# Optimization experiments

Hardware: AMD Instinct MI355X
Metric: run time of the kernel (lower is better)

The kernel has to match this reference:

```python
import jax, jax.numpy as jnp
import numpy as np

MARGIN = 0.2
W_HARD = 1.0
W_SOFT = 0.0
NORMALIZE = True
PD_EPS = 1e-6  # torch F.pairwise_distance eps used inside TripletMarginLoss


def setup_inputs() -> dict:
    key = jax.random.key(0)
    k1, k2, k3 = jax.random.split(key, 3)
    N, D = 8192, 128
    z = jax.random.normal(k1, (N, D), dtype=jnp.float32)
    labels = jax.random.randint(k2, (N,), 0, 16, dtype=jnp.int32)
    subjects = jax.random.randint(k3, (N,), 0, 32, dtype=jnp.int32)
    return {"z": z, "labels": labels, "subjects": subjects}


def _batch_hard(z, pos_mask, neg_mask, margin):
    # pairwise euclidean distances (cdist p=2); mining indices are ints, so
    # stop_gradient keeps vjp clean (matches torch: argmax/argmin detach).
    sq = jnp.sum(z * z, axis=1)
    d2 = sq[:, None] + sq[None, :] - 2.0 * (z @ z.T)
    dist = jax.lax.stop_gradient(jnp.sqrt(jnp.maximum(d2, 0.0)))
    inf = jnp.asarray(jnp.inf, dist.dtype)
    p_idx = jnp.argmax(jnp.where(pos_mask, dist, -inf), axis=1)  # hardest positive
    n_idx = jnp.argmin(jnp.where(neg_mask, dist, inf), axis=1)   # hardest negative
    valid = jnp.any(pos_mask, axis=1) & jnp.any(neg_mask, axis=1)
    a, p, n = z, z[p_idx], z[n_idx]
    d_ap = jnp.sqrt(jnp.sum((a - p + PD_EPS) ** 2, axis=1))
    d_an = jnp.sqrt(jnp.sum((a - n + PD_EPS) ** 2, axis=1))
    per = jnp.maximum(d_ap - d_an + margin, 0.0)
    cnt = jnp.sum(valid)
    loss = jnp.sum(per * valid) / jnp.maximum(cnt, 1).astype(per.dtype)
    return jnp.where(cnt > 0, loss, 0.0)


def reference(z, labels, subjects):
    if NORMALIZE:
        z = z / jnp.maximum(jnp.linalg.norm(z, axis=1, keepdims=True), 1e-12)
    N = z.shape[0]
    same_class = labels[:, None] == labels[None, :]
    same_subj = subjects[:, None] == subjects[None, :]
    not_eye = ~jnp.eye(N, dtype=bool)
    loss = 0.0
    denom = 0.0
    if W_HARD != 0:
        pos_hard = same_class & ~same_subj & not_eye
        neg_hard = ~same_class & same_subj & not_eye
        loss = loss + W_HARD * _batch_hard(z, pos_hard, neg_hard, MARGIN)
        denom += abs(W_HARD)
    if W_SOFT != 0:
        pos_soft = same_class & same_subj & not_eye
        neg_soft = ~same_class & ~same_subj & not_eye
        loss = loss + W_SOFT * _batch_hard(z, pos_soft, neg_soft, MARGIN)
        denom += abs(W_SOFT)
    return loss / max(denom, 1e-12)
```

## Files before the change

### kernel.cpp

```cpp
#include <hip/hip_runtime.h>
#include <math.h>

#define N 8192
#define D 128
#define MARGIN 0.2f
#define PD_EPS 1e-6f
#define CLS_STRIDE 1024
#define SUB_STRIDE 512

typedef __attribute__((ext_vector_type(8))) short bf16x8;
typedef __attribute__((ext_vector_type(4))) float f32x4;

__device__ __forceinline__ unsigned short f2bf(float f) {
    unsigned u = __float_as_uint(f);
    u += 0x7FFFu + ((u >> 16) & 1u);
    return (unsigned short)(u >> 16);
}
__device__ __forceinline__ unsigned umn(unsigned a, unsigned b) { return a < b ? a : b; }
__device__ __forceinline__ unsigned umx(unsigned a, unsigned b) { return a > b ? a : b; }

__global__ __launch_bounds__(256) void k_normalize(const float* __restrict__ z,
                                                   unsigned short* __restrict__ znb,
                                                   float* __restrict__ invn) {
    int row  = blockIdx.x * 4 + (threadIdx.x >> 6);
    int lane = threadIdx.x & 63;
    float2 v = ((const float2*)(z + (size_t)row * D))[lane];
    float ss = v.x * v.x + v.y * v.y;
    #pragma unroll
    for (int m = 1; m < 64; m <<= 1) ss += __shfl_xor(ss, m, 64);
    float norm = fmaxf(sqrtf(ss), 1e-12f);
    ushort2 b; b.x = f2bf(v.x / norm); b.y = f2bf(v.y / norm);
    ((ushort2*)(znb + (size_t)row * D))[lane] = b;
    if (lane == 0) invn[row] = 1.0f / norm;
}

__global__ __launch_bounds__(1024) void k_bucket(const int* __restrict__ labels,
                                                 const int* __restrict__ subjects,
                                                 int* __restrict__ counters,
                                                 int* __restrict__ clsIdx,
                                                 int* __restrict__ subIdx,
                                                 float* __restrict__ acc) {
    __shared__ int hc[16], hs[32];
    const int t = threadIdx.x;
    if (t < 16) hc[t] = 0;
    if (t < 32) hs[t] = 0;
    if (t < 3)  acc[t] = 0.0f;
    __syncthreads();
    #pragma unroll
    for (int r = 0; r < 8; ++r) {
        int row = r * 1024 + t;
        int lab = labels[row], sub = subjects[row];
        int rc = atomicAdd(&hc[lab], 1);
        if (rc < CLS_STRIDE) clsIdx[lab * CLS_STRIDE + rc] = (sub << 13) | row;
        int rs = atomicAdd(&hs[sub], 1);
        if (rs < SUB_STRIDE) subIdx[sub * SUB_STRIDE + rs] = (lab << 13) | row;
    }
    __syncthreads();
    if (t < 16) counters[t] = hc[t];
    else if (t < 48) counters[t] = hs[t - 16];
}

__global__ __launch_bounds__(64, 2) void k_mine(const unsigned short* __restrict__ znb,
                                                const int* __restrict__ counters,
                                                const int* __restrict__ clsIdx,
                                                const int* __restrict__ subIdx,
                                                unsigned* __restrict__ posk,
                                                unsigned* __restrict__ negk) {
    const int b = blockIdx.x;
    const bool isPos = b < 256;
    const int* idx; int cnt, atile;
    if (isPos) {
        int c = b >> 4; atile = b & 15;
        idx = clsIdx + c * CLS_STRIDE;
        cnt = min(counters[c], CLS_STRIDE);
    } else {
        int t = b - 256; int su = t >> 3; atile = t & 7;
        idx = subIdx + su * SUB_STRIDE;
        cnt = min(counters[16 + su], SUB_STRIDE);
    }
    if (atile * 64 >= cnt) return;

    const int lane = threadIdx.x;
    const int m = lane & 15, quad = lane >> 4;

    bf16x8 afrag[4][4];
    #pragma unroll
    for (int u = 0; u < 4; ++u) {
        int sl = min(atile * 64 + u * 16 + m, cnt - 1);
        size_t row = (size_t)(idx[sl] & 8191);
        #pragma unroll
        for (int s = 0; s < 4; ++s)
            afrag[u][s] = *(const bf16x8*)(znb + row * D + s * 32 + quad * 8);
    }
    int cpk[16];
    #pragma unroll
    for (int u = 0; u < 4; ++u)
        #pragma unroll
        for (int r = 0; r < 4; ++r)
            cpk[u * 4 + r] = idx[min(atile * 64 + u * 16 + quad * 4 + r, cnt - 1)];

    unsigned best[16];
    #pragma unroll
    for (int s = 0; s < 16; ++s) best[s] = isPos ? 0xFFFFFFFFu : 0u;

    const int njt = (cnt + 63) >> 6;
    for (int t = 0; t < njt; ++t) {
        int pkB[4];
        #pragma unroll
        for (int v = 0; v < 4; ++v)
            pkB[v] = idx[min(t * 64 + v * 16 + m, cnt - 1)];

        f32x4 acc[4][4];
        #pragma unroll
        for (int u = 0; u < 4; ++u)
            #pragma unroll
            for (int v = 0; v < 4; ++v)
                acc[u][v] = (f32x4){0.f, 0.f, 0.f, 0.f};

        #pragma unroll
        for (int s = 0; s < 4; ++s) {
            bf16x8 bf[4];
            #pragma unroll
            for (int v = 0; v < 4; ++v)
                bf[v] = *(const bf16x8*)(znb + (size_t)(pkB[v] & 8191) * D + s * 32 + quad * 8);
            #pragma unroll
            for (int u = 0; u < 4; ++u)
                #pragma unroll
                for (int v = 0; v < 4; ++v)
                    acc[u][v] = __builtin_amdgcn_mfma_f32_16x16x32_bf16(afrag[u][s], bf[v], acc[u][v], 0, 0, 0);
        }

        #pragma unroll
        for (int v = 0; v < 4; ++v) {
            const unsigned pj = (unsigned)pkB[v];
            #pragma unroll
            for (int u = 0; u < 4; ++u)
                #pragma unroll
                for (int r = 0; r < 4; ++r) {
                    const int s16 = u * 4 + r;
                    unsigned key = (__float_as_uint(acc[u][v][r] + 2.0f) & 0xFFFFE000u) | (pj & 8191u);
                    bool sel = (((unsigned)cpk[s16] ^ pj) & 0xFFFFE000u) != 0u;
                    if (isPos) best[s16] = umn(best[s16], sel ? key : 0xFFFFFFFFu);
                    else       best[s16] = umx(best[s16], sel ? key : 0u);
                }
        }
    }

    #pragma unroll
    for (int mm = 1; mm < 16; mm <<= 1)
        #pragma unroll
        for (int s = 0; s < 16; ++s) {
            unsigned o = (unsigned)__shfl_xor((int)best[s], mm, 64);
            best[s] = isPos ? umn(best[s], o) : umx(best[s], o);
        }
    if (m == 0) {
        unsigned* dst = isPos ? posk : negk;
        #pragma unroll
        for (int s = 0; s < 16; ++s)
            dst[cpk[s] & 8191] = best[s];
    }
}

__global__ __launch_bounds__(256) void k_final(const float* __restrict__ z,
                                               const float* __restrict__ invn,
                                               const unsigned* __restrict__ posk,
                                               const unsigned* __restrict__ negk,
                                               float* __restrict__ acc,
                                               float* __restrict__ out) {
    const int rb = threadIdx.x >> 4;
    const int l  = threadIdx.x & 15;
    const int row = blockIdx.x * 16 + rb;
    unsigned mp = posk[row], mn = negk[row];
    bool valid = (mp != 0xFFFFFFFFu) && (mn != 0u);
    int pi = valid ? (int)(mp & 8191u) : 0;
    int ni = valid ? (int)(mn & 8191u) : 0;
    float ia = invn[row], ip = invn[pi], iq = invn[ni];
    const float4* za = (const float4*)(z + (size_t)row * D);
    const float4* zp = (const float4*)(z + (size_t)pi * D);
    const float4* zq = (const float4*)(z + (size_t)ni * D);
    float sap = 0.f, san = 0.f;
    #pragma unroll
    for (int k = 0; k < 2; ++k) {
        float4 a = za[l * 2 + k], p = zp[l * 2 + k], q = zq[l * 2 + k];
        float d;
        d = a.x * ia - p.x * ip + PD_EPS; sap += d * d;
        d = a.y * ia - p.y * ip + PD_EPS; sap += d * d;
        d = a.z * ia - p.z * ip + PD_EPS; sap += d * d;
        d = a.w * ia - p.w * ip + PD_EPS; sap += d * d;
        d = a.x * ia - q.x * iq + PD_EPS; san += d * d;
        d = a.y * ia - q.y * iq + PD_EPS; san += d * d;
        d = a.z * ia - q.z * iq + PD_EPS; san += d * d;
        d = a.w * ia - q.w * iq + PD_EPS; san += d * d;
    }
    #pragma unroll
    for (int mm = 1; mm < 16; mm <<= 1) {
        sap += __shfl_xor(sap, mm, 64);
        san += __shfl_xor(san, mm, 64);
    }
    __shared__ float ls[16], vs[16];
    if (l == 0) {
        float lo = fmaxf(sqrtf(sap) - sqrtf(san) + MARGIN, 0.0f);
        ls[rb] = valid ? lo : 0.0f;
        vs[rb] = valid ? 1.0f : 0.0f;
    }
    __syncthreads();
    if (threadIdx.x == 0) {
        float s = 0.f, c = 0.f;
        #pragma unroll
        for (int i = 0; i < 16; ++i) { s += ls[i]; c += vs[i]; }
        atomicAdd(&acc[0], s);
        atomicAdd(&acc[1], c);
        __threadfence();
        unsigned old = atomicAdd((unsigned*)&acc[2], 1u);
        if (old == (unsigned)(gridDim.x - 1)) {
            float S = atomicAdd(&acc[0], 0.0f);
            float C = atomicAdd(&acc[1], 0.0f);
            out[0] = (C > 0.f) ? S / fmaxf(C, 1.f) : 0.f;
        }
    }
}

extern "C" void kernel_launch(void* const* d_in, const int* in_sizes, int n_in,
                              void* d_out, int out_size, void* d_ws, size_t ws_size,
                              hipStream_t stream) {
    const float* z        = (const float*)d_in[0];
    const int*   labels   = (const int*)d_in[1];
    const int*   subjects = (const int*)d_in[2];
    float* out = (float*)d_out;

    char* ws = (char*)d_ws;
    unsigned short* znb  = (unsigned short*)(ws);
    float*    invn     = (float*)   (ws + 2097152);
    int*      clsIdx   = (int*)     (ws + 2129920);
    int*      subIdx   = (int*)     (ws + 2195456);
    unsigned* posk     = (unsigned*)(ws + 2260992);
    unsigned* negk     = (unsigned*)(ws + 2293760);
    int*      counters = (int*)     (ws + 2326528);
    float*    acc      = (float*)   (ws + 2326528 + 48 * 4);

    k_normalize<<<dim3(N / 4), dim3(256), 0, stream>>>(z, znb, invn);
    k_bucket<<<dim3(1), dim3(1024), 0, stream>>>(labels, subjects, counters, clsIdx, subIdx, acc);
    k_mine<<<dim3(512), dim3(64), 0, stream>>>(znb, counters, clsIdx, subIdx, posk, negk);
    k_final<<<dim3(N / 16), dim3(256), 0, stream>>>(z, invn, posk, negk, acc, out);
}
```

Measured before the change: 121.3 us.

## Fuse normalize and bucketing into one launch with per-bucket ballot compaction

```diff
diff --git a/kernel.cpp b/kernel.cpp
--- a/kernel.cpp
+++ b/kernel.cpp
@@ -19,45 +19,61 @@
 __device__ __forceinline__ unsigned umn(unsigned a, unsigned b) { return a < b ? a : b; }
 __device__ __forceinline__ unsigned umx(unsigned a, unsigned b) { return a > b ? a : b; }
 
-__global__ __launch_bounds__(256) void k_normalize(const float* __restrict__ z,
-                                                   unsigned short* __restrict__ znb,
-                                                   float* __restrict__ invn) {
-    int row  = blockIdx.x * 4 + (threadIdx.x >> 6);
-    int lane = threadIdx.x & 63;
-    float2 v = ((const float2*)(z + (size_t)row * D))[lane];
-    float ss = v.x * v.x + v.y * v.y;
-    #pragma unroll
-    for (int m = 1; m < 64; m <<= 1) ss += __shfl_xor(ss, m, 64);
-    float norm = fmaxf(sqrtf(ss), 1e-12f);
-    ushort2 b; b.x = f2bf(v.x / norm); b.y = f2bf(v.y / norm);
-    ((ushort2*)(znb + (size_t)row * D))[lane] = b;
-    if (lane == 0) invn[row] = 1.0f / norm;
-}
-
-__global__ __launch_bounds__(1024) void k_bucket(const int* __restrict__ labels,
-                                                 const int* __restrict__ subjects,
-                                                 int* __restrict__ counters,
-                                                 int* __restrict__ clsIdx,
-                                                 int* __restrict__ subIdx,
-                                                 float* __restrict__ acc) {
-    __shared__ int hc[16], hs[32];
+__global__ __launch_bounds__(256) void k_norm_bucket(const float* __restrict__ z,
+                                                     const int* __restrict__ labels,
+                                                     const int* __restrict__ subjects,
+                                                     unsigned short* __restrict__ znb,
+                                                     float* __restrict__ invn,
+                                                     int* __restrict__ counters,
+                                                     int* __restrict__ clsIdx,
+                                                     int* __restrict__ subIdx,
+                                                     float* __restrict__ acc) {
+    const int b = blockIdx.x;
     const int t = threadIdx.x;
-    if (t < 16) hc[t] = 0;
-    if (t < 32) hs[t] = 0;
-    if (t < 3)  acc[t] = 0.0f;
-    __syncthreads();
-    #pragma unroll
-    for (int r = 0; r < 8; ++r) {
-        int row = r * 1024 + t;
-        int lab = labels[row], sub = subjects[row];
-        int rc = atomicAdd(&hc[lab], 1);
-        if (rc < CLS_STRIDE) clsIdx[lab * CLS_STRIDE + rc] = (sub << 13) | row;
-        int rs = atomicAdd(&hs[sub], 1);
-        if (rs < SUB_STRIDE) subIdx[sub * SUB_STRIDE + rs] = (lab << 13) | row;
-    }
-    __syncthreads();
-    if (t < 16) counters[t] = hc[t];
-    else if (t < 48) counters[t] = hs[t - 16];
+    if (b < 48) {
+        const bool isCls = b < 16;
+        const int  tgt   = isCls ? b : b - 16;
+        const int  wave  = t >> 6, lane = t & 63;
+        __shared__ int wbase[4];
+        __shared__ int blkbase;
+        if (t == 0) blkbase = 0;
+        if (b == 0 && t < 3) acc[t] = 0.0f;
+        __syncthreads();
+        int* dst = isCls ? (clsIdx + tgt * CLS_STRIDE) : (subIdx + tgt * SUB_STRIDE);
+        const int stride = isCls ? CLS_STRIDE : SUB_STRIDE;
+        for (int base = 0; base < N; base += 256) {
+            int row = base + t;
+            int lab = labels[row], sub = subjects[row];
+            int key   = isCls ? lab : sub;
+            int other = isCls ? sub : lab;
+            bool pred = (key == tgt);
+            unsigned long long mask = __ballot(pred);
+            int lrank = __popcll(mask & ((1ull << lane) - 1ull));
+            if (lane == 0) wbase[wave] = __popcll(mask);
+            __syncthreads();
+            int wb = 0;
+            #pragma unroll
+            for (int w = 0; w < 4; ++w) if (w < wave) wb += wbase[w];
+            int chunktot = wbase[0] + wbase[1] + wbase[2] + wbase[3];
+            int pos = blkbase + wb + lrank;
+            if (pred && pos < stride) dst[pos] = (other << 13) | row;
+            __syncthreads();
+            if (t == 0) blkbase += chunktot;
+        }
+        __syncthreads();
+        if (t == 0) counters[isCls ? tgt : 16 + tgt] = blkbase;
+    } else {
+        int row  = (b - 48) * 4 + (t >> 6);
+        int lane = t & 63;
+        float2 v = ((const float2*)(z + (size_t)row * D))[lane];
+        float ss = v.x * v.x + v.y * v.y;
+        #pragma unroll
+        for (int m = 1; m < 64; m <<= 1) ss += __shfl_xor(ss, m, 64);
+        float norm = fmaxf(sqrtf(ss), 1e-12f);
+        ushort2 bb; bb.x = f2bf(v.x / norm); bb.y = f2bf(v.y / norm);
+        ((ushort2*)(znb + (size_t)row * D))[lane] = bb;
+        if (lane == 0) invn[row] = 1.0f / norm;
+    }
 }
 
 __global__ __launch_bounds__(64, 2) void k_mine(const unsigned short* __restrict__ znb,
@@ -238,8 +254,8 @@
     int*      counters = (int*)     (ws + 2326528);
     float*    acc      = (float*)   (ws + 2326528 + 48 * 4);
 
-    k_normalize<<<dim3(N / 4), dim3(256), 0, stream>>>(z, znb, invn);
-    k_bucket<<<dim3(1), dim3(1024), 0, stream>>>(labels, subjects, counters, clsIdx, subIdx, acc);
+    k_norm_bucket<<<dim3(48 + N / 4), dim3(256), 0, stream>>>(z, labels, subjects, znb, invn,
+                                                              counters, clsIdx, subIdx, acc);
     k_mine<<<dim3(512), dim3(64), 0, stream>>>(znb, counters, clsIdx, subIdx, posk, negk);
     k_final<<<dim3(N / 16), dim3(256), 0, stream>>>(z, invn, posk, negk, acc, out);
 }
```

New measurement: 125.2 us. +3.2%, slower.
